# Performance work log

Measured on AMD Instinct MI355X. Metric: run time of the kernel, lower is better.

The kernel has to match this reference:

```python
import jax, jax.numpy as jnp
import numpy as np

N_NODES = 100000

def _sage_conv(x, src, dst, W_l, b_l, W_r):
    # PyG SAGEConv(aggr='mean'): out = lin_l(mean_{j in N(i)} x_j) + lin_r(x_i)
    agg = jax.ops.segment_sum(x[src], dst, num_segments=N_NODES)          # [N, F]
    cnt = jax.ops.segment_sum(jnp.ones_like(dst, dtype=x.dtype), dst,
                              num_segments=N_NODES)                        # [N]
    mean = agg / jnp.maximum(cnt, 1.0)[:, None]
    return mean @ W_l + b_l + x @ W_r

def setup_inputs() -> dict:
    key = jax.random.key(0)
    ks = jax.random.split(key, 10)
    F_in, H = 128, 16
    E, P = 1600000, 2000000
    x = jax.random.normal(ks[0], (N_NODES, F_in), dtype=jnp.float32)
    edge_index = jax.random.randint(ks[1], (2, E), 0, N_NODES, dtype=jnp.int64)
    decode_index = jax.random.randint(ks[2], (2, P), 0, N_NODES, dtype=jnp.int64)
    s1 = 1.0 / np.sqrt(F_in)
    s2 = 1.0 / np.sqrt(H)
    W1l = jax.random.uniform(ks[3], (F_in, H), jnp.float32, -s1, s1)
    b1 = jax.random.uniform(ks[4], (H,), jnp.float32, -s1, s1)
    W1r = jax.random.uniform(ks[5], (F_in, H), jnp.float32, -s1, s1)
    W2l = jax.random.uniform(ks[6], (H, H), jnp.float32, -s2, s2)
    b2 = jax.random.uniform(ks[7], (H,), jnp.float32, -s2, s2)
    W2r = jax.random.uniform(ks[8], (H, H), jnp.float32, -s2, s2)
    return {"x": x, "W1l": W1l, "b1": b1, "W1r": W1r,
            "W2l": W2l, "b2": b2, "W2r": W2r,
            "edge_index": edge_index, "decode_index": decode_index}

def reference(x, W1l, b1, W1r, W2l, b2, W2r, edge_index, decode_index):
    src, dst = edge_index[0], edge_index[1]
    h = _sage_conv(x, src, dst, W1l, b1, W1r)          # conv1
    h = jax.nn.relu(h)                                  # relu (dropout: eval -> identity)
    h = _sage_conv(h, src, dst, W2l, b2, W2r)           # conv2
    logits = jnp.sum(h[decode_index[0]] * h[decode_index[1]], axis=1)  # [P]
    return jax.nn.sigmoid(logits)
```

## Files before the change

### kernel.cpp

```cpp
#include <hip/hip_runtime.h>
#include <hip/hip_fp16.h>

#define N_NODES 100000
#define F_IN 128
#define H 16
#define NBIN 391
#define BINCAP 4608
#define ECHUNK 8192
#define QSCALE 4096.0f
#define QINV (1.0f / 4096.0f)

__device__ inline unsigned int packi16(float a, float b) {
  int ia = __float2int_rn(fminf(fmaxf(a * QSCALE, -32767.f), 32767.f));
  int ib = __float2int_rn(fminf(fmaxf(b * QSCALE, -32767.f), 32767.f));
  return (unsigned int)((ia & 0xffff) | (ib << 16));
}

__device__ inline unsigned long long pk64(unsigned int w) {
  return ((unsigned long long)((w >> 16) ^ 0x8000u) << 32)
       | (unsigned long long)((w & 0xffffu) ^ 0x8000u);
}

__global__ void __launch_bounds__(512) k_init(int* __restrict__ binCur) {
  int t = threadIdx.x;
  if (t < NBIN) binCur[t] = t * BINCAP;
}

__global__ void __launch_bounds__(512) k_front(
    const float* __restrict__ x, const float* __restrict__ W1l,
    const float* __restrict__ W1r, unsigned short* __restrict__ y1l,
    float* __restrict__ y1r,
    const int* __restrict__ src, const int* __restrict__ dst,
    int* __restrict__ binCur, int* __restrict__ recs, int E, int fillB) {
  __shared__ __align__(16) char smem[49152];
  int t = threadIdx.x;
  int b = blockIdx.x;
  if (b < fillB) {
    int* hist = (int*)smem;
    int* gbase = hist + 512;
    int* cnt2 = gbase + 512;
    hist[t] = 0;
    cnt2[t] = 0;
    __syncthreads();
    int base = b * ECHUNK;
    int rec[16], bin[16];
#pragma unroll
    for (int j = 0; j < 16; ++j) {
      int e = base + j * 512 + t;
      if (e < E) {
        int s = src[e];
        int d = dst[e];
        rec[j] = (s << 8) | (d & 255);
        bin[j] = d >> 8;
        atomicAdd(&hist[bin[j]], 1);
      } else {
        bin[j] = -1;
      }
    }
    __syncthreads();
    if (t < NBIN) {
      int c = hist[t];
      gbase[t] = (c > 0) ? atomicAdd(&binCur[t], c) : 0;
    }
    __syncthreads();
#pragma unroll
    for (int j = 0; j < 16; ++j) {
      if (bin[j] >= 0) {
        int loc = atomicAdd(&cnt2[bin[j]], 1);
        int slot = gbase[bin[j]] + loc;
        if (slot < (bin[j] + 1) * BINCAP)
          recs[slot] = rec[j];
      }
    }
  } else {
    int lb = b - fillB;
    int wid = __builtin_amdgcn_readfirstlane(t >> 6);
    int part = wid & 3;
    int g = wid >> 2;
    int ln = t & 63;
    int n = lb * 128 + g * 64 + ln;
    int nc = (n < N_NODES) ? n : (N_NODES - 1);
    float* red = (float*)smem + g * 6144;
    const float4* xr = (const float4*)(x + (size_t)nc * F_IN + part * (F_IN / 4));
    float4 xv[8];
#pragma unroll
    for (int j = 0; j < 8; ++j) xv[j] = xr[j];
    const float* Wl = W1l + part * (F_IN / 4) * H;
    const float* Wr = W1r + part * (F_IN / 4) * H;
    float al[H], ar[H];
#pragma unroll
    for (int c = 0; c < H; ++c) { al[c] = 0.f; ar[c] = 0.f; }
#pragma unroll
    for (int j = 0; j < 8; ++j) {
      float xs[4] = {xv[j].x, xv[j].y, xv[j].z, xv[j].w};
#pragma unroll
      for (int jj = 0; jj < 4; ++jj) {
        int k = j * 4 + jj;
#pragma unroll
        for (int c = 0; c < H; ++c) {
          al[c] = fmaf(xs[jj], Wl[k * H + c], al[c]);
          ar[c] = fmaf(xs[jj], Wr[k * H + c], ar[c]);
        }
      }
    }
    if (part != 0) {
      int base = (part - 1) * 2048;
#pragma unroll
      for (int c = 0; c < H; ++c) {
        red[base + c * 64 + ln] = al[c];
        red[base + (H + c) * 64 + ln] = ar[c];
      }
    }
    __syncthreads();
    if (part == 0 && n < N_NODES) {
#pragma unroll
      for (int c = 0; c < H; ++c) {
        al[c] = ((al[c] + red[c * 64 + ln]) + red[2048 + c * 64 + ln])
                + red[4096 + c * 64 + ln];
        ar[c] = ((ar[c] + red[(H + c) * 64 + ln]) + red[2048 + (H + c) * 64 + ln])
                + red[4096 + (H + c) * 64 + ln];
      }
      uint4 w0, w1;
      w0.x = packi16(al[0], al[1]);  w0.y = packi16(al[2], al[3]);
      w0.z = packi16(al[4], al[5]);  w0.w = packi16(al[6], al[7]);
      w1.x = packi16(al[8], al[9]);  w1.y = packi16(al[10], al[11]);
      w1.z = packi16(al[12], al[13]); w1.w = packi16(al[14], al[15]);
      uint4* ol = (uint4*)(y1l + (size_t)n * H);
      ol[0] = w0;
      ol[1] = w1;
      float4* orr = (float4*)(y1r + (size_t)n * H);
#pragma unroll
      for (int q = 0; q < 4; ++q)
        orr[q] = make_float4(ar[4 * q], ar[4 * q + 1], ar[4 * q + 2], ar[4 * q + 3]);
    }
  }
}

__global__ void __launch_bounds__(512) k_agg1(
    const int* __restrict__ recs, const int* __restrict__ binCur,
    const unsigned short* __restrict__ y1l, const float* __restrict__ y1r,
    const float* __restrict__ b1, const float* __restrict__ W2l,
    const float* __restrict__ W2r, unsigned short* __restrict__ z2l,
    float* __restrict__ z2r) {
  __shared__ unsigned long long acc[8][256];
  __shared__ int cnt[256];
  __shared__ float hf[16][256];
  __shared__ float w2l[256];
  __shared__ float w2r[256];
  int t = threadIdx.x;
  int b = blockIdx.x;
#pragma unroll
  for (int j = 0; j < 4; ++j) ((unsigned long long*)acc)[j * 512 + t] = 0ULL;
  if (t < 256) { cnt[t] = 0; w2l[t] = W2l[t]; }
  else         w2r[t - 256] = W2r[t - 256];
  __syncthreads();
  int rbase = b * BINCAP;
  int R = binCur[b] - rbase;
  if (R > BINCAP) R = BINCAP;
  int rr[9];
#pragma unroll
  for (int j = 0; j < 9; ++j) {
    int idx = j * 512 + t;
    rr[j] = (idx < R) ? recs[rbase + idx] : -1;
  }
  uint4 va[9], vb[9];
#pragma unroll
  for (int j = 0; j < 9; ++j) {
    int s = (rr[j] >= 0) ? (rr[j] >> 8) : 0;
    const uint4* yp = (const uint4*)(y1l + (size_t)s * H);
    va[j] = yp[0];
    vb[j] = yp[1];
  }
#pragma unroll
  for (int j = 0; j < 9; ++j) {
    if (rr[j] >= 0) {
      int nb = rr[j] & 255;
      uint4 v0 = va[j], v1 = vb[j];
      atomicAdd(&cnt[nb], 1);
      atomicAdd(&acc[0][nb], pk64(v0.x));
      atomicAdd(&acc[1][nb], pk64(v0.y));
      atomicAdd(&acc[2][nb], pk64(v0.z));
      atomicAdd(&acc[3][nb], pk64(v0.w));
      atomicAdd(&acc[4][nb], pk64(v1.x));
      atomicAdd(&acc[5][nb], pk64(v1.y));
      atomicAdd(&acc[6][nb], pk64(v1.z));
      atomicAdd(&acc[7][nb], pk64(v1.w));
    }
  }
  __syncthreads();
  int node = t >> 1;
  int half = t & 1;
  int coff = half * 8;
  int n = (b << 8) + node;
  if (n < N_NODES) {
    int dg = cnt[node];
    unsigned int bias = (unsigned int)dg << 15;
    float s = QINV / fmaxf((float)dg, 1.f);
    const float4* yrp = (const float4*)(y1r + (size_t)n * H + coff);
    float4 y0 = yrp[0], y1v = yrp[1];
    const float4* bp = (const float4*)(b1 + coff);
    float4 b0 = bp[0], b1v = bp[1];
    float yv[8] = {y0.x, y0.y, y0.z, y0.w, y1v.x, y1v.y, y1v.z, y1v.w};
    float bv[8] = {b0.x, b0.y, b0.z, b0.w, b1v.x, b1v.y, b1v.z, b1v.w};
    int ia[8];
#pragma unroll
    for (int p = 0; p < 4; ++p) {
      unsigned long long a = acc[half * 4 + p][node];
      ia[2 * p]     = (int)((unsigned int)a - bias);
      ia[2 * p + 1] = (int)((unsigned int)(a >> 32) - bias);
    }
#pragma unroll
    for (int c = 0; c < 8; ++c) {
      float h = fmaf((float)ia[c], s, bv[c] + yv[c]);
      hf[coff + c][node] = fmaxf(h, 0.f);
    }
  } else {
#pragma unroll
    for (int c = 0; c < 8; ++c) hf[coff + c][node] = 0.f;
  }
  __syncthreads();
  float zl[8], zr[8];
#pragma unroll
  for (int c = 0; c < 8; ++c) { zl[c] = 0.f; zr[c] = 0.f; }
#pragma unroll
  for (int k = 0; k < 16; ++k) {
    float hk = hf[k][node];
#pragma unroll
    for (int c = 0; c < 8; ++c) {
      zl[c] = fmaf(hk, w2l[k * 16 + coff + c], zl[c]);
      zr[c] = fmaf(hk, w2r[k * 16 + coff + c], zr[c]);
    }
  }
  if (n < N_NODES) {
    uint4 pk;
    pk.x = packi16(zl[0], zl[1]);
    pk.y = packi16(zl[2], zl[3]);
    pk.z = packi16(zl[4], zl[5]);
    pk.w = packi16(zl[6], zl[7]);
    *(uint4*)(z2l + (size_t)n * H + coff) = pk;
    float4* zp = (float4*)(z2r + (size_t)n * H + coff);
    zp[0] = make_float4(zr[0], zr[1], zr[2], zr[3]);
    zp[1] = make_float4(zr[4], zr[5], zr[6], zr[7]);
  }
}

__global__ void __launch_bounds__(512) k_agg2(
    const int* __restrict__ recs, const int* __restrict__ binCur,
    const unsigned short* __restrict__ z2l, const float* __restrict__ z2r,
    const float* __restrict__ b2, __half* __restrict__ h2) {
  __shared__ unsigned long long acc[8][256];
  __shared__ int cnt[256];
  int t = threadIdx.x;
  int b = blockIdx.x;
#pragma unroll
  for (int j = 0; j < 4; ++j) ((unsigned long long*)acc)[j * 512 + t] = 0ULL;
  if (t < 256) cnt[t] = 0;
  __syncthreads();
  int rbase = b * BINCAP;
  int R = binCur[b] - rbase;
  if (R > BINCAP) R = BINCAP;
  int rr[9];
#pragma unroll
  for (int j = 0; j < 9; ++j) {
    int idx = j * 512 + t;
    rr[j] = (idx < R) ? recs[rbase + idx] : -1;
  }
  uint4 va[9], vb[9];
#pragma unroll
  for (int j = 0; j < 9; ++j) {
    int s = (rr[j] >= 0) ? (rr[j] >> 8) : 0;
    const uint4* yp = (const uint4*)(z2l + (size_t)s * H);
    va[j] = yp[0];
    vb[j] = yp[1];
  }
#pragma unroll
  for (int j = 0; j < 9; ++j) {
    if (rr[j] >= 0) {
      int nb = rr[j] & 255;
      uint4 v0 = va[j], v1 = vb[j];
      atomicAdd(&cnt[nb], 1);
      atomicAdd(&acc[0][nb], pk64(v0.x));
      atomicAdd(&acc[1][nb], pk64(v0.y));
      atomicAdd(&acc[2][nb], pk64(v0.z));
      atomicAdd(&acc[3][nb], pk64(v0.w));
      atomicAdd(&acc[4][nb], pk64(v1.x));
      atomicAdd(&acc[5][nb], pk64(v1.y));
      atomicAdd(&acc[6][nb], pk64(v1.z));
      atomicAdd(&acc[7][nb], pk64(v1.w));
    }
  }
  __syncthreads();
  int node = t >> 1;
  int half = t & 1;
  int coff = half * 8;
  int n = (b << 8) + node;
  if (n < N_NODES) {
    int dg = cnt[node];
    unsigned int bias = (unsigned int)dg << 15;
    float s = QINV / fmaxf((float)dg, 1.f);
    const float4* zrp = (const float4*)(z2r + (size_t)n * H + coff);
    float4 z0 = zrp[0], z1 = zrp[1];
    const float4* bp = (const float4*)(b2 + coff);
    float4 b0 = bp[0], b1v = bp[1];
    float zv[8] = {z0.x, z0.y, z0.z, z0.w, z1.x, z1.y, z1.z, z1.w};
    float bv[8] = {b0.x, b0.y, b0.z, b0.w, b1v.x, b1v.y, b1v.z, b1v.w};
    int ia[8];
#pragma unroll
    for (int p = 0; p < 4; ++p) {
      unsigned long long a = acc[half * 4 + p][node];
      ia[2 * p]     = (int)((unsigned int)a - bias);
      ia[2 * p + 1] = (int)((unsigned int)(a >> 32) - bias);
    }
    float v[8];
#pragma unroll
    for (int c = 0; c < 8; ++c)
      v[c] = fmaf((float)ia[c], s, bv[c] + zv[c]);
    __half2 h0 = __floats2half2_rn(v[0], v[1]);
    __half2 h1 = __floats2half2_rn(v[2], v[3]);
    __half2 h2p = __floats2half2_rn(v[4], v[5]);
    __half2 h3 = __floats2half2_rn(v[6], v[7]);
    uint4 pk;
    pk.x = *(unsigned int*)&h0;
    pk.y = *(unsigned int*)&h1;
    pk.z = *(unsigned int*)&h2p;
    pk.w = *(unsigned int*)&h3;
    *(uint4*)(h2 + (size_t)n * H + coff) = pk;
  }
}

__device__ inline float dot8h(uint4 u, uint4 v) {
  float acc = 0.f;
  const unsigned int* uw = (const unsigned int*)&u;
  const unsigned int* vw = (const unsigned int*)&v;
#pragma unroll
  for (int j = 0; j < 4; ++j) {
    float2 a = __half22float2(*(const __half2*)&uw[j]);
    float2 b = __half22float2(*(const __half2*)&vw[j]);
    acc = fmaf(a.x, b.x, acc);
    acc = fmaf(a.y, b.y, acc);
  }
  return acc;
}

__global__ void __launch_bounds__(256) k_decode(
    const int* __restrict__ ps, const int* __restrict__ pd,
    const __half* __restrict__ h2, float* __restrict__ out, int P) {
  int t = blockIdx.x * 256 + threadIdx.x;
  int p = t * 2;
  if (p >= P) return;
  int2 av = *(const int2*)(ps + p);
  int2 bv = *(const int2*)(pd + p);
  const uint4* ha0 = (const uint4*)(h2 + (size_t)av.x * H);
  const uint4* hb0 = (const uint4*)(h2 + (size_t)bv.x * H);
  const uint4* ha1 = (const uint4*)(h2 + (size_t)av.y * H);
  const uint4* hb1 = (const uint4*)(h2 + (size_t)bv.y * H);
  uint4 u00 = ha0[0], u01 = ha0[1];
  uint4 v00 = hb0[0], v01 = hb0[1];
  uint4 u10 = ha1[0], u11 = ha1[1];
  uint4 v10 = hb1[0], v11 = hb1[1];
  float d0 = dot8h(u00, v00) + dot8h(u01, v01);
  float d1 = dot8h(u10, v10) + dot8h(u11, v11);
  float o0 = 1.f / (1.f + __expf(-d0));
  float o1 = 1.f / (1.f + __expf(-d1));
  if (p + 1 < P) {
    *(float2*)(out + p) = make_float2(o0, o1);
  } else {
    out[p] = o0;
  }
}

extern "C" void kernel_launch(void* const* d_in, const int* in_sizes, int n_in,
                              void* d_out, int out_size, void* d_ws, size_t ws_size,
                              hipStream_t stream) {
  const float* x   = (const float*)d_in[0];
  const float* W1l = (const float*)d_in[1];
  const float* b1  = (const float*)d_in[2];
  const float* W1r = (const float*)d_in[3];
  const float* W2l = (const float*)d_in[4];
  const float* b2  = (const float*)d_in[5];
  const float* W2r = (const float*)d_in[6];
  const int* ei = (const int*)d_in[7];
  const int* di = (const int*)d_in[8];
  const int E = in_sizes[7] / 2;
  const int P = in_sizes[8] / 2;

  const size_t NF = (size_t)N_NODES * H;
  unsigned short* y1l = (unsigned short*)d_ws;
  __half*         h2  = (__half*)y1l;
  unsigned short* z2l = y1l + NF;
  float*  y1r = (float*)(z2l + NF);
  float*  z2r = y1r;
  int* recs   = (int*)(y1r + NF);
  int* binCur = recs + (size_t)NBIN * BINCAP;

  const int fillB = (E + ECHUNK - 1) / ECHUNK;
  const int lin1B = (N_NODES + 127) / 128;
  const int decodeBlocks = ((P + 1) / 2 + 255) / 256;

  k_init<<<1, 512, 0, stream>>>(binCur);
  k_front<<<fillB + lin1B, 512, 0, stream>>>(x, W1l, W1r, y1l, y1r,
                                             ei, ei + E, binCur, recs, E, fillB);
  k_agg1<<<NBIN, 512, 0, stream>>>(recs, binCur, y1l, y1r, b1, W2l, W2r,
                                   z2l, z2r);
  k_agg2<<<NBIN, 512, 0, stream>>>(recs, binCur, z2l, z2r, b2, h2);
  k_decode<<<decodeBlocks, 256, 0, stream>>>(di, di + P, h2, (float*)d_out, P);
}
```

Measured before the change: 197.6 us.

## Fuse all stages into one persistent kernel with software grid barriers

Replaces the four separate stage kernels (front/bin-fill, agg1, agg2, decode) with one persistent kernel of 391 blocks that moves between stages using atomic-counter grid barriers. Edge binning and the first linear layer run as grid-stride loops within the same blocks. The register-held gather batches in the aggregation stages are processed in chunks of three to lower register pressure under the tighter launch bounds. This removes kernel launch gaps and tail effects, but relies on all 391 blocks being co-resident and limits the decode and front phases to a fixed block count.

```diff
diff --git a/kernel.cpp b/kernel.cpp
--- a/kernel.cpp
+++ b/kernel.cpp
@@ -6,7 +6,8 @@
 #define H 16
 #define NBIN 391
 #define BINCAP 4608
-#define ECHUNK 8192
+#define NBLK 391
+#define FCHUNK 4096
 #define QSCALE 4096.0f
 #define QINV (1.0f / 4096.0f)
 
@@ -21,351 +22,401 @@
        | (unsigned long long)((w & 0xffffu) ^ 0x8000u);
 }
 
-__global__ void __launch_bounds__(512) k_init(int* __restrict__ binCur) {
+__device__ inline void grid_sync(int* cnt, int* gen) {
+  __syncthreads();
+  if (threadIdx.x == 0) {
+    __threadfence();
+    int g = __hip_atomic_load(gen, __ATOMIC_RELAXED, __HIP_MEMORY_SCOPE_AGENT);
+    int v = __hip_atomic_fetch_add(cnt, 1, __ATOMIC_ACQ_REL,
+                                   __HIP_MEMORY_SCOPE_AGENT);
+    if (v == NBLK - 1) {
+      __hip_atomic_store(cnt, 0, __ATOMIC_RELAXED, __HIP_MEMORY_SCOPE_AGENT);
+      __hip_atomic_fetch_add(gen, 1, __ATOMIC_RELEASE,
+                             __HIP_MEMORY_SCOPE_AGENT);
+    } else {
+      while (__hip_atomic_load(gen, __ATOMIC_ACQUIRE,
+                               __HIP_MEMORY_SCOPE_AGENT) == g)
+        __builtin_amdgcn_s_sleep(8);
+    }
+    __threadfence();
+  }
+  __syncthreads();
+}
+
+__global__ void __launch_bounds__(1024) k_init(int* __restrict__ binCur) {
   int t = threadIdx.x;
-  if (t < NBIN) binCur[t] = t * BINCAP;
-}
-
-__global__ void __launch_bounds__(512) k_front(
+  binCur[t] = (t < 512) ? t * BINCAP : 0;
+}
+
+__global__ void __launch_bounds__(512, 4) k_mega(
     const float* __restrict__ x, const float* __restrict__ W1l,
-    const float* __restrict__ W1r, unsigned short* __restrict__ y1l,
-    float* __restrict__ y1r,
-    const int* __restrict__ src, const int* __restrict__ dst,
-    int* __restrict__ binCur, int* __restrict__ recs, int E, int fillB) {
+    const float* __restrict__ W1r, const float* __restrict__ b1,
+    const float* __restrict__ W2l, const float* __restrict__ W2r,
+    const float* __restrict__ b2, const int* __restrict__ src,
+    const int* __restrict__ dst, const int* __restrict__ ps,
+    const int* __restrict__ pd, unsigned short* y1l,
+    unsigned short* z2l, float* y1r, int* recs, int* binCur,
+    float* __restrict__ out, int E, int P) {
   __shared__ __align__(16) char smem[49152];
   int t = threadIdx.x;
   int b = blockIdx.x;
-  if (b < fillB) {
+  int* barCnt = binCur + 544;
+  int* barGen = binCur + 576;
+
+  {
     int* hist = (int*)smem;
     int* gbase = hist + 512;
     int* cnt2 = gbase + 512;
-    hist[t] = 0;
-    cnt2[t] = 0;
-    __syncthreads();
-    int base = b * ECHUNK;
-    int rec[16], bin[16];
-#pragma unroll
-    for (int j = 0; j < 16; ++j) {
-      int e = base + j * 512 + t;
-      if (e < E) {
-        int s = src[e];
-        int d = dst[e];
-        rec[j] = (s << 8) | (d & 255);
-        bin[j] = d >> 8;
-        atomicAdd(&hist[bin[j]], 1);
-      } else {
-        bin[j] = -1;
-      }
-    }
-    __syncthreads();
-    if (t < NBIN) {
-      int c = hist[t];
-      gbase[t] = (c > 0) ? atomicAdd(&binCur[t], c) : 0;
-    }
-    __syncthreads();
-#pragma unroll
-    for (int j = 0; j < 16; ++j) {
-      if (bin[j] >= 0) {
-        int loc = atomicAdd(&cnt2[bin[j]], 1);
-        int slot = gbase[bin[j]] + loc;
-        if (slot < (bin[j] + 1) * BINCAP)
-          recs[slot] = rec[j];
-      }
-    }
-  } else {
-    int lb = b - fillB;
+    int nchunks = (E + FCHUNK - 1) / FCHUNK;
+    for (int c = b; c < nchunks; c += NBLK) {
+      hist[t] = 0;
+      cnt2[t] = 0;
+      __syncthreads();
+      int base = c * FCHUNK;
+      int rec[8], bin[8];
+#pragma unroll
+      for (int j = 0; j < 8; ++j) {
+        int e = base + j * 512 + t;
+        if (e < E) {
+          int s = src[e];
+          int d = dst[e];
+          rec[j] = (s << 8) | (d & 255);
+          bin[j] = d >> 8;
+          atomicAdd(&hist[bin[j]], 1);
+        } else {
+          bin[j] = -1;
+        }
+      }
+      __syncthreads();
+      if (t < NBIN) {
+        int cc = hist[t];
+        gbase[t] = (cc > 0) ? atomicAdd(&binCur[t], cc) : 0;
+      }
+      __syncthreads();
+#pragma unroll
+      for (int j = 0; j < 8; ++j) {
+        if (bin[j] >= 0) {
+          int loc = atomicAdd(&cnt2[bin[j]], 1);
+          int slot = gbase[bin[j]] + loc;
+          if (slot < (bin[j] + 1) * BINCAP)
+            recs[slot] = rec[j];
+        }
+      }
+      __syncthreads();
+    }
+  }
+  __syncthreads();
+
+  {
     int wid = __builtin_amdgcn_readfirstlane(t >> 6);
     int part = wid & 3;
     int g = wid >> 2;
     int ln = t & 63;
-    int n = lb * 128 + g * 64 + ln;
-    int nc = (n < N_NODES) ? n : (N_NODES - 1);
     float* red = (float*)smem + g * 6144;
-    const float4* xr = (const float4*)(x + (size_t)nc * F_IN + part * (F_IN / 4));
-    float4 xv[8];
-#pragma unroll
-    for (int j = 0; j < 8; ++j) xv[j] = xr[j];
-    const float* Wl = W1l + part * (F_IN / 4) * H;
-    const float* Wr = W1r + part * (F_IN / 4) * H;
-    float al[H], ar[H];
-#pragma unroll
-    for (int c = 0; c < H; ++c) { al[c] = 0.f; ar[c] = 0.f; }
-#pragma unroll
-    for (int j = 0; j < 8; ++j) {
-      float xs[4] = {xv[j].x, xv[j].y, xv[j].z, xv[j].w};
-#pragma unroll
-      for (int jj = 0; jj < 4; ++jj) {
-        int k = j * 4 + jj;
+#pragma unroll 1
+    for (int tile = b; tile < 782; tile += NBLK) {
+      int n = tile * 128 + g * 64 + ln;
+      int nc = (n < N_NODES) ? n : (N_NODES - 1);
+      const float4* xr =
+          (const float4*)(x + (size_t)nc * F_IN + part * (F_IN / 4));
+      float4 xv[8];
+#pragma unroll
+      for (int j = 0; j < 8; ++j) xv[j] = xr[j];
+      const float* Wl = W1l + part * (F_IN / 4) * H;
+      const float* Wr = W1r + part * (F_IN / 4) * H;
+      float al[H], ar[H];
+#pragma unroll
+      for (int c = 0; c < H; ++c) { al[c] = 0.f; ar[c] = 0.f; }
+#pragma unroll
+      for (int j = 0; j < 8; ++j) {
+        float xs[4] = {xv[j].x, xv[j].y, xv[j].z, xv[j].w};
+#pragma unroll
+        for (int jj = 0; jj < 4; ++jj) {
+          int k = j * 4 + jj;
+#pragma unroll
+          for (int c = 0; c < H; ++c) {
+            al[c] = fmaf(xs[jj], Wl[k * H + c], al[c]);
+            ar[c] = fmaf(xs[jj], Wr[k * H + c], ar[c]);
+          }
+        }
+      }
+      if (part != 0) {
+        int base = (part - 1) * 2048;
 #pragma unroll
         for (int c = 0; c < H; ++c) {
-          al[c] = fmaf(xs[jj], Wl[k * H + c], al[c]);
-          ar[c] = fmaf(xs[jj], Wr[k * H + c], ar[c]);
-        }
-      }
-    }
-    if (part != 0) {
-      int base = (part - 1) * 2048;
-#pragma unroll
-      for (int c = 0; c < H; ++c) {
-        red[base + c * 64 + ln] = al[c];
-        red[base + (H + c) * 64 + ln] = ar[c];
-      }
-    }
+          red[base + c * 64 + ln] = al[c];
+          red[base + (H + c) * 64 + ln] = ar[c];
+        }
+      }
+      __syncthreads();
+      if (part == 0 && n < N_NODES) {
+#pragma unroll
+        for (int c = 0; c < H; ++c) {
+          al[c] = ((al[c] + red[c * 64 + ln]) + red[2048 + c * 64 + ln])
+                  + red[4096 + c * 64 + ln];
+          ar[c] = ((ar[c] + red[(H + c) * 64 + ln])
+                   + red[2048 + (H + c) * 64 + ln])
+                  + red[4096 + (H + c) * 64 + ln];
+        }
+        uint4 w0, w1;
+        w0.x = packi16(al[0], al[1]);  w0.y = packi16(al[2], al[3]);
+        w0.z = packi16(al[4], al[5]);  w0.w = packi16(al[6], al[7]);
+        w1.x = packi16(al[8], al[9]);  w1.y = packi16(al[10], al[11]);
+        w1.z = packi16(al[12], al[13]); w1.w = packi16(al[14], al[15]);
+        uint4* ol = (uint4*)(y1l + (size_t)n * H);
+        ol[0] = w0;
+        ol[1] = w1;
+        float4* orr = (float4*)(y1r + (size_t)n * H);
+#pragma unroll
+        for (int q = 0; q < 4; ++q)
+          orr[q] = make_float4(ar[4 * q], ar[4 * q + 1], ar[4 * q + 2],
+                               ar[4 * q + 3]);
+      }
+      __syncthreads();
+    }
+  }
+  grid_sync(barCnt, barGen);
+
+  {
+    unsigned long long (*acc)[256] = (unsigned long long (*)[256])smem;
+    int* cnt = (int*)(smem + 16384);
+    float (*hf)[256] = (float (*)[256])(smem + 17408);
+    float* w2l = (float*)(smem + 33792);
+    float* w2r = (float*)(smem + 34816);
+#pragma unroll
+    for (int j = 0; j < 4; ++j) ((unsigned long long*)acc)[j * 512 + t] = 0ULL;
+    if (t < 256) { cnt[t] = 0; w2l[t] = W2l[t]; }
+    else         w2r[t - 256] = W2r[t - 256];
     __syncthreads();
-    if (part == 0 && n < N_NODES) {
-#pragma unroll
-      for (int c = 0; c < H; ++c) {
-        al[c] = ((al[c] + red[c * 64 + ln]) + red[2048 + c * 64 + ln])
-                + red[4096 + c * 64 + ln];
-        ar[c] = ((ar[c] + red[(H + c) * 64 + ln]) + red[2048 + (H + c) * 64 + ln])
-                + red[4096 + (H + c) * 64 + ln];
-      }
-      uint4 w0, w1;
-      w0.x = packi16(al[0], al[1]);  w0.y = packi16(al[2], al[3]);
-      w0.z = packi16(al[4], al[5]);  w0.w = packi16(al[6], al[7]);
-      w1.x = packi16(al[8], al[9]);  w1.y = packi16(al[10], al[11]);
-      w1.z = packi16(al[12], al[13]); w1.w = packi16(al[14], al[15]);
-      uint4* ol = (uint4*)(y1l + (size_t)n * H);
-      ol[0] = w0;
-      ol[1] = w1;
-      float4* orr = (float4*)(y1r + (size_t)n * H);
-#pragma unroll
-      for (int q = 0; q < 4; ++q)
-        orr[q] = make_float4(ar[4 * q], ar[4 * q + 1], ar[4 * q + 2], ar[4 * q + 3]);
-    }
-  }
-}
-
-__global__ void __launch_bounds__(512) k_agg1(
-    const int* __restrict__ recs, const int* __restrict__ binCur,
-    const unsigned short* __restrict__ y1l, const float* __restrict__ y1r,
-    const float* __restrict__ b1, const float* __restrict__ W2l,
-    const float* __restrict__ W2r, unsigned short* __restrict__ z2l,
-    float* __restrict__ z2r) {
-  __shared__ unsigned long long acc[8][256];
-  __shared__ int cnt[256];
-  __shared__ float hf[16][256];
-  __shared__ float w2l[256];
-  __shared__ float w2r[256];
-  int t = threadIdx.x;
-  int b = blockIdx.x;
-#pragma unroll
-  for (int j = 0; j < 4; ++j) ((unsigned long long*)acc)[j * 512 + t] = 0ULL;
-  if (t < 256) { cnt[t] = 0; w2l[t] = W2l[t]; }
-  else         w2r[t - 256] = W2r[t - 256];
-  __syncthreads();
-  int rbase = b * BINCAP;
-  int R = binCur[b] - rbase;
-  if (R > BINCAP) R = BINCAP;
-  int rr[9];
-#pragma unroll
-  for (int j = 0; j < 9; ++j) {
-    int idx = j * 512 + t;
-    rr[j] = (idx < R) ? recs[rbase + idx] : -1;
-  }
-  uint4 va[9], vb[9];
-#pragma unroll
-  for (int j = 0; j < 9; ++j) {
-    int s = (rr[j] >= 0) ? (rr[j] >> 8) : 0;
-    const uint4* yp = (const uint4*)(y1l + (size_t)s * H);
-    va[j] = yp[0];
-    vb[j] = yp[1];
-  }
-#pragma unroll
-  for (int j = 0; j < 9; ++j) {
-    if (rr[j] >= 0) {
-      int nb = rr[j] & 255;
-      uint4 v0 = va[j], v1 = vb[j];
-      atomicAdd(&cnt[nb], 1);
-      atomicAdd(&acc[0][nb], pk64(v0.x));
-      atomicAdd(&acc[1][nb], pk64(v0.y));
-      atomicAdd(&acc[2][nb], pk64(v0.z));
-      atomicAdd(&acc[3][nb], pk64(v0.w));
-      atomicAdd(&acc[4][nb], pk64(v1.x));
-      atomicAdd(&acc[5][nb], pk64(v1.y));
-      atomicAdd(&acc[6][nb], pk64(v1.z));
-      atomicAdd(&acc[7][nb], pk64(v1.w));
-    }
-  }
-  __syncthreads();
-  int node = t >> 1;
-  int half = t & 1;
-  int coff = half * 8;
-  int n = (b << 8) + node;
-  if (n < N_NODES) {
-    int dg = cnt[node];
-    unsigned int bias = (unsigned int)dg << 15;
-    float s = QINV / fmaxf((float)dg, 1.f);
-    const float4* yrp = (const float4*)(y1r + (size_t)n * H + coff);
-    float4 y0 = yrp[0], y1v = yrp[1];
-    const float4* bp = (const float4*)(b1 + coff);
-    float4 b0 = bp[0], b1v = bp[1];
-    float yv[8] = {y0.x, y0.y, y0.z, y0.w, y1v.x, y1v.y, y1v.z, y1v.w};
-    float bv[8] = {b0.x, b0.y, b0.z, b0.w, b1v.x, b1v.y, b1v.z, b1v.w};
-    int ia[8];
-#pragma unroll
-    for (int p = 0; p < 4; ++p) {
-      unsigned long long a = acc[half * 4 + p][node];
-      ia[2 * p]     = (int)((unsigned int)a - bias);
-      ia[2 * p + 1] = (int)((unsigned int)(a >> 32) - bias);
-    }
-#pragma unroll
-    for (int c = 0; c < 8; ++c) {
-      float h = fmaf((float)ia[c], s, bv[c] + yv[c]);
-      hf[coff + c][node] = fmaxf(h, 0.f);
-    }
-  } else {
-#pragma unroll
-    for (int c = 0; c < 8; ++c) hf[coff + c][node] = 0.f;
-  }
-  __syncthreads();
-  float zl[8], zr[8];
-#pragma unroll
-  for (int c = 0; c < 8; ++c) { zl[c] = 0.f; zr[c] = 0.f; }
-#pragma unroll
-  for (int k = 0; k < 16; ++k) {
-    float hk = hf[k][node];
-#pragma unroll
-    for (int c = 0; c < 8; ++c) {
-      zl[c] = fmaf(hk, w2l[k * 16 + coff + c], zl[c]);
-      zr[c] = fmaf(hk, w2r[k * 16 + coff + c], zr[c]);
-    }
-  }
-  if (n < N_NODES) {
-    uint4 pk;
-    pk.x = packi16(zl[0], zl[1]);
-    pk.y = packi16(zl[2], zl[3]);
-    pk.z = packi16(zl[4], zl[5]);
-    pk.w = packi16(zl[6], zl[7]);
-    *(uint4*)(z2l + (size_t)n * H + coff) = pk;
-    float4* zp = (float4*)(z2r + (size_t)n * H + coff);
-    zp[0] = make_float4(zr[0], zr[1], zr[2], zr[3]);
-    zp[1] = make_float4(zr[4], zr[5], zr[6], zr[7]);
-  }
-}
-
-__global__ void __launch_bounds__(512) k_agg2(
-    const int* __restrict__ recs, const int* __restrict__ binCur,
-    const unsigned short* __restrict__ z2l, const float* __restrict__ z2r,
-    const float* __restrict__ b2, __half* __restrict__ h2) {
-  __shared__ unsigned long long acc[8][256];
-  __shared__ int cnt[256];
-  int t = threadIdx.x;
-  int b = blockIdx.x;
-#pragma unroll
-  for (int j = 0; j < 4; ++j) ((unsigned long long*)acc)[j * 512 + t] = 0ULL;
-  if (t < 256) cnt[t] = 0;
-  __syncthreads();
-  int rbase = b * BINCAP;
-  int R = binCur[b] - rbase;
-  if (R > BINCAP) R = BINCAP;
-  int rr[9];
-#pragma unroll
-  for (int j = 0; j < 9; ++j) {
-    int idx = j * 512 + t;
-    rr[j] = (idx < R) ? recs[rbase + idx] : -1;
-  }
-  uint4 va[9], vb[9];
-#pragma unroll
-  for (int j = 0; j < 9; ++j) {
-    int s = (rr[j] >= 0) ? (rr[j] >> 8) : 0;
-    const uint4* yp = (const uint4*)(z2l + (size_t)s * H);
-    va[j] = yp[0];
-    vb[j] = yp[1];
-  }
-#pragma unroll
-  for (int j = 0; j < 9; ++j) {
-    if (rr[j] >= 0) {
-      int nb = rr[j] & 255;
-      uint4 v0 = va[j], v1 = vb[j];
-      atomicAdd(&cnt[nb], 1);
-      atomicAdd(&acc[0][nb], pk64(v0.x));
-      atomicAdd(&acc[1][nb], pk64(v0.y));
-      atomicAdd(&acc[2][nb], pk64(v0.z));
-      atomicAdd(&acc[3][nb], pk64(v0.w));
-      atomicAdd(&acc[4][nb], pk64(v1.x));
-      atomicAdd(&acc[5][nb], pk64(v1.y));
-      atomicAdd(&acc[6][nb], pk64(v1.z));
-      atomicAdd(&acc[7][nb], pk64(v1.w));
-    }
-  }
-  __syncthreads();
-  int node = t >> 1;
-  int half = t & 1;
-  int coff = half * 8;
-  int n = (b << 8) + node;
-  if (n < N_NODES) {
-    int dg = cnt[node];
-    unsigned int bias = (unsigned int)dg << 15;
-    float s = QINV / fmaxf((float)dg, 1.f);
-    const float4* zrp = (const float4*)(z2r + (size_t)n * H + coff);
-    float4 z0 = zrp[0], z1 = zrp[1];
-    const float4* bp = (const float4*)(b2 + coff);
-    float4 b0 = bp[0], b1v = bp[1];
-    float zv[8] = {z0.x, z0.y, z0.z, z0.w, z1.x, z1.y, z1.z, z1.w};
-    float bv[8] = {b0.x, b0.y, b0.z, b0.w, b1v.x, b1v.y, b1v.z, b1v.w};
-    int ia[8];
-#pragma unroll
-    for (int p = 0; p < 4; ++p) {
-      unsigned long long a = acc[half * 4 + p][node];
-      ia[2 * p]     = (int)((unsigned int)a - bias);
-      ia[2 * p + 1] = (int)((unsigned int)(a >> 32) - bias);
-    }
-    float v[8];
-#pragma unroll
-    for (int c = 0; c < 8; ++c)
-      v[c] = fmaf((float)ia[c], s, bv[c] + zv[c]);
-    __half2 h0 = __floats2half2_rn(v[0], v[1]);
-    __half2 h1 = __floats2half2_rn(v[2], v[3]);
-    __half2 h2p = __floats2half2_rn(v[4], v[5]);
-    __half2 h3 = __floats2half2_rn(v[6], v[7]);
-    uint4 pk;
-    pk.x = *(unsigned int*)&h0;
-    pk.y = *(unsigned int*)&h1;
-    pk.z = *(unsigned int*)&h2p;
-    pk.w = *(unsigned int*)&h3;
-    *(uint4*)(h2 + (size_t)n * H + coff) = pk;
-  }
-}
-
-__device__ inline float dot8h(uint4 u, uint4 v) {
-  float acc = 0.f;
-  const unsigned int* uw = (const unsigned int*)&u;
-  const unsigned int* vw = (const unsigned int*)&v;
-#pragma unroll
-  for (int j = 0; j < 4; ++j) {
-    float2 a = __half22float2(*(const __half2*)&uw[j]);
-    float2 b = __half22float2(*(const __half2*)&vw[j]);
-    acc = fmaf(a.x, b.x, acc);
-    acc = fmaf(a.y, b.y, acc);
-  }
-  return acc;
-}
-
-__global__ void __launch_bounds__(256) k_decode(
-    const int* __restrict__ ps, const int* __restrict__ pd,
-    const __half* __restrict__ h2, float* __restrict__ out, int P) {
-  int t = blockIdx.x * 256 + threadIdx.x;
-  int p = t * 2;
-  if (p >= P) return;
-  int2 av = *(const int2*)(ps + p);
-  int2 bv = *(const int2*)(pd + p);
-  const uint4* ha0 = (const uint4*)(h2 + (size_t)av.x * H);
-  const uint4* hb0 = (const uint4*)(h2 + (size_t)bv.x * H);
-  const uint4* ha1 = (const uint4*)(h2 + (size_t)av.y * H);
-  const uint4* hb1 = (const uint4*)(h2 + (size_t)bv.y * H);
-  uint4 u00 = ha0[0], u01 = ha0[1];
-  uint4 v00 = hb0[0], v01 = hb0[1];
-  uint4 u10 = ha1[0], u11 = ha1[1];
-  uint4 v10 = hb1[0], v11 = hb1[1];
-  float d0 = dot8h(u00, v00) + dot8h(u01, v01);
-  float d1 = dot8h(u10, v10) + dot8h(u11, v11);
-  float o0 = 1.f / (1.f + __expf(-d0));
-  float o1 = 1.f / (1.f + __expf(-d1));
-  if (p + 1 < P) {
-    *(float2*)(out + p) = make_float2(o0, o1);
-  } else {
-    out[p] = o0;
+    int rbase = b * BINCAP;
+    int R = binCur[b] - rbase;
+    if (R > BINCAP) R = BINCAP;
+#pragma unroll 1
+    for (int c0 = 0; c0 < 9; c0 += 3) {
+      int rc[3];
+      uint4 va[3], vb[3];
+#pragma unroll
+      for (int jj = 0; jj < 3; ++jj) {
+        int idx = (c0 + jj) * 512 + t;
+        rc[jj] = (idx < R) ? recs[rbase + idx] : -1;
+      }
+#pragma unroll
+      for (int jj = 0; jj < 3; ++jj) {
+        int s = (rc[jj] >= 0) ? (rc[jj] >> 8) : 0;
+        const uint4* yp = (const uint4*)(y1l + (size_t)s * H);
+        va[jj] = yp[0];
+        vb[jj] = yp[1];
+      }
+#pragma unroll
+      for (int jj = 0; jj < 3; ++jj) {
+        if (rc[jj] >= 0) {
+          int nb = rc[jj] & 255;
+          atomicAdd(&cnt[nb], 1);
+          atomicAdd(&acc[0][nb], pk64(va[jj].x));
+          atomicAdd(&acc[1][nb], pk64(va[jj].y));
+          atomicAdd(&acc[2][nb], pk64(va[jj].z));
+          atomicAdd(&acc[3][nb], pk64(va[jj].w));
+          atomicAdd(&acc[4][nb], pk64(vb[jj].x));
+          atomicAdd(&acc[5][nb], pk64(vb[jj].y));
+          atomicAdd(&acc[6][nb], pk64(vb[jj].z));
+          atomicAdd(&acc[7][nb], pk64(vb[jj].w));
+        }
+      }
+    }
+    __syncthreads();
+    int node = t >> 1;
+    int half = t & 1;
+    int coff = half * 8;
+    int n = (b << 8) + node;
+    if (n < N_NODES) {
+      int dg = cnt[node];
+      unsigned int bias = (unsigned int)dg << 15;
+      float s = QINV / fmaxf((float)dg, 1.f);
+      const float4* yrp = (const float4*)(y1r + (size_t)n * H + coff);
+      float4 y0 = yrp[0], y1v = yrp[1];
+      const float4* bp = (const float4*)(b1 + coff);
+      float4 b0 = bp[0], b1v = bp[1];
+      float yv[8] = {y0.x, y0.y, y0.z, y0.w, y1v.x, y1v.y, y1v.z, y1v.w};
+      float bv[8] = {b0.x, b0.y, b0.z, b0.w, b1v.x, b1v.y, b1v.z, b1v.w};
+      int ia[8];
+#pragma unroll
+      for (int p = 0; p < 4; ++p) {
+        unsigned long long a = acc[half * 4 + p][node];
+        ia[2 * p]     = (int)((unsigned int)a - bias);
+        ia[2 * p + 1] = (int)((unsigned int)(a >> 32) - bias);
+      }
+#pragma unroll
+      for (int c = 0; c < 8; ++c) {
+        float h = fmaf((float)ia[c], s, bv[c] + yv[c]);
+        hf[coff + c][node] = fmaxf(h, 0.f);
+      }
+    } else {
+#pragma unroll
+      for (int c = 0; c < 8; ++c) hf[coff + c][node] = 0.f;
+    }
+    __syncthreads();
+    float zl[8], zr[8];
+#pragma unroll
+    for (int c = 0; c < 8; ++c) { zl[c] = 0.f; zr[c] = 0.f; }
+#pragma unroll
+    for (int k = 0; k < 16; ++k) {
+      float hk = hf[k][node];
+#pragma unroll
+      for (int c = 0; c < 8; ++c) {
+        zl[c] = fmaf(hk, w2l[k * 16 + coff + c], zl[c]);
+        zr[c] = fmaf(hk, w2r[k * 16 + coff + c], zr[c]);
+      }
+    }
+    if (n < N_NODES) {
+      uint4 pk;
+      pk.x = packi16(zl[0], zl[1]);
+      pk.y = packi16(zl[2], zl[3]);
+      pk.z = packi16(zl[4], zl[5]);
+      pk.w = packi16(zl[6], zl[7]);
+      *(uint4*)(z2l + (size_t)n * H + coff) = pk;
+      float4* zp = (float4*)(y1r + (size_t)n * H + coff);
+      zp[0] = make_float4(zr[0], zr[1], zr[2], zr[3]);
+      zp[1] = make_float4(zr[4], zr[5], zr[6], zr[7]);
+    }
+  }
+  grid_sync(barCnt, barGen);
+
+  {
+    unsigned long long (*acc)[256] = (unsigned long long (*)[256])smem;
+    int* cnt = (int*)(smem + 16384);
+#pragma unroll
+    for (int j = 0; j < 4; ++j) ((unsigned long long*)acc)[j * 512 + t] = 0ULL;
+    if (t < 256) cnt[t] = 0;
+    __syncthreads();
+    int rbase = b * BINCAP;
+    int R = binCur[b] - rbase;
+    if (R > BINCAP) R = BINCAP;
+#pragma unroll 1
+    for (int c0 = 0; c0 < 9; c0 += 3) {
+      int rc[3];
+      uint4 va[3], vb[3];
+#pragma unroll
+      for (int jj = 0; jj < 3; ++jj) {
+        int idx = (c0 + jj) * 512 + t;
+        rc[jj] = (idx < R) ? recs[rbase + idx] : -1;
+      }
+#pragma unroll
+      for (int jj = 0; jj < 3; ++jj) {
+        int s = (rc[jj] >= 0) ? (rc[jj] >> 8) : 0;
+        const uint4* yp = (const uint4*)(z2l + (size_t)s * H);
+        va[jj] = yp[0];
+        vb[jj] = yp[1];
+      }
+#pragma unroll
+      for (int jj = 0; jj < 3; ++jj) {
+        if (rc[jj] >= 0) {
+          int nb = rc[jj] & 255;
+          atomicAdd(&cnt[nb], 1);
+          atomicAdd(&acc[0][nb], pk64(va[jj].x));
+          atomicAdd(&acc[1][nb], pk64(va[jj].y));
+          atomicAdd(&acc[2][nb], pk64(va[jj].z));
+          atomicAdd(&acc[3][nb], pk64(va[jj].w));
+          atomicAdd(&acc[4][nb], pk64(vb[jj].x));
+          atomicAdd(&acc[5][nb], pk64(vb[jj].y));
+          atomicAdd(&acc[6][nb], pk64(vb[jj].z));
+          atomicAdd(&acc[7][nb], pk64(vb[jj].w));
+        }
+      }
+    }
+    __syncthreads();
+    int node = t >> 1;
+    int half = t & 1;
+    int coff = half * 8;
+    int n = (b << 8) + node;
+    if (n < N_NODES) {
+      int dg = cnt[node];
+      unsigned int bias = (unsigned int)dg << 15;
+      float s = QINV / fmaxf((float)dg, 1.f);
+      const float4* zrp = (const float4*)(y1r + (size_t)n * H + coff);
+      float4 z0 = zrp[0], z1 = zrp[1];
+      const float4* bp = (const float4*)(b2 + coff);
+      float4 b0 = bp[0], b1v = bp[1];
+      float zv[8] = {z0.x, z0.y, z0.z, z0.w, z1.x, z1.y, z1.z, z1.w};
+      float bv[8] = {b0.x, b0.y, b0.z, b0.w, b1v.x, b1v.y, b1v.z, b1v.w};
+      int ia[8];
+#pragma unroll
+      for (int p = 0; p < 4; ++p) {
+        unsigned long long a = acc[half * 4 + p][node];
+        ia[2 * p]     = (int)((unsigned int)a - bias);
+        ia[2 * p + 1] = (int)((unsigned int)(a >> 32) - bias);
+      }
+      float v[8];
+#pragma unroll
+      for (int c = 0; c < 8; ++c)
+        v[c] = fmaf((float)ia[c], s, bv[c] + zv[c]);
+      __half2 h0 = __floats2half2_rn(v[0], v[1]);
+      __half2 h1 = __floats2half2_rn(v[2], v[3]);
+      __half2 hh2 = __floats2half2_rn(v[4], v[5]);
+      __half2 h3 = __floats2half2_rn(v[6], v[7]);
+      uint4 pk;
+      pk.x = *(unsigned int*)&h0;
+      pk.y = *(unsigned int*)&h1;
+      pk.z = *(unsigned int*)&hh2;
+      pk.w = *(unsigned int*)&h3;
+      *(uint4*)((__half*)y1l + (size_t)n * H + coff) = pk;
+    }
+  }
+  grid_sync(barCnt, barGen);
+
+  {
+    const __half* h2 = (const __half*)y1l;
+    const int tp = NBLK * 512;
+    for (int u = b * 512 + t; 2 * u < P; u += tp) {
+      int p = 2 * u;
+      int2 av = *(const int2*)(ps + p);
+      int2 bv = *(const int2*)(pd + p);
+      const uint4* ha0 = (const uint4*)(h2 + (size_t)av.x * H);
+      const uint4* hb0 = (const uint4*)(h2 + (size_t)bv.x * H);
+      const uint4* ha1 = (const uint4*)(h2 + (size_t)av.y * H);
+      const uint4* hb1 = (const uint4*)(h2 + (size_t)bv.y * H);
+      uint4 u00 = ha0[0], u01 = ha0[1];
+      uint4 v00 = hb0[0], v01 = hb0[1];
+      uint4 u10 = ha1[0], u11 = ha1[1];
+      uint4 v10 = hb1[0], v11 = hb1[1];
+      float d0 = 0.f, d1 = 0.f;
+      const unsigned int* uw;
+      const unsigned int* vw;
+      uw = (const unsigned int*)&u00; vw = (const unsigned int*)&v00;
+#pragma unroll
+      for (int j = 0; j < 4; ++j) {
+        float2 a = __half22float2(*(const __half2*)&uw[j]);
+        float2 bb = __half22float2(*(const __half2*)&vw[j]);
+        d0 = fmaf(a.x, bb.x, d0); d0 = fmaf(a.y, bb.y, d0);
+      }
+      uw = (const unsigned int*)&u01; vw = (const unsigned int*)&v01;
+#pragma unroll
+      for (int j = 0; j < 4; ++j) {
+        float2 a = __half22float2(*(const __half2*)&uw[j]);
+        float2 bb = __half22float2(*(const __half2*)&vw[j]);
+        d0 = fmaf(a.x, bb.x, d0); d0 = fmaf(a.y, bb.y, d0);
+      }
+      uw = (const unsigned int*)&u10; vw = (const unsigned int*)&v10;
+#pragma unroll
+      for (int j = 0; j < 4; ++j) {
+        float2 a = __half22float2(*(const __half2*)&uw[j]);
+        float2 bb = __half22float2(*(const __half2*)&vw[j]);
+        d1 = fmaf(a.x, bb.x, d1); d1 = fmaf(a.y, bb.y, d1);
+      }
+      uw = (const unsigned int*)&u11; vw = (const unsigned int*)&v11;
+#pragma unroll
+      for (int j = 0; j < 4; ++j) {
+        float2 a = __half22float2(*(const __half2*)&uw[j]);
+        float2 bb = __half22float2(*(const __half2*)&vw[j]);
+        d1 = fmaf(a.x, bb.x, d1); d1 = fmaf(a.y, bb.y, d1);
+      }
+      float o0 = 1.f / (1.f + __expf(-d0));
+      float o1 = 1.f / (1.f + __expf(-d1));
+      if (p + 1 < P) {
+        *(float2*)(out + p) = make_float2(o0, o1);
+      } else {
+        out[p] = o0;
+      }
+    }
   }
 }
 
@@ -386,22 +437,14 @@
 
   const size_t NF = (size_t)N_NODES * H;
   unsigned short* y1l = (unsigned short*)d_ws;
-  __half*         h2  = (__half*)y1l;
   unsigned short* z2l = y1l + NF;
   float*  y1r = (float*)(z2l + NF);
-  float*  z2r = y1r;
   int* recs   = (int*)(y1r + NF);
   int* binCur = recs + (size_t)NBIN * BINCAP;
 
-  const int fillB = (E + ECHUNK - 1) / ECHUNK;
-  const int lin1B = (N_NODES + 127) / 128;
-  const int decodeBlocks = ((P + 1) / 2 + 255) / 256;
-
-  k_init<<<1, 512, 0, stream>>>(binCur);
-  k_front<<<fillB + lin1B, 512, 0, stream>>>(x, W1l, W1r, y1l, y1r,
-                                             ei, ei + E, binCur, recs, E, fillB);
-  k_agg1<<<NBIN, 512, 0, stream>>>(recs, binCur, y1l, y1r, b1, W2l, W2r,
-                                   z2l, z2r);
-  k_agg2<<<NBIN, 512, 0, stream>>>(recs, binCur, z2l, z2r, b2, h2);
-  k_decode<<<decodeBlocks, 256, 0, stream>>>(di, di + P, h2, (float*)d_out, P);
-}
+  k_init<<<1, 1024, 0, stream>>>(binCur);
+  k_mega<<<NBLK, 512, 0, stream>>>(x, W1l, W1r, b1, W2l, W2r, b2,
+                                   ei, ei + E, di, di + P,
+                                   y1l, z2l, y1r, recs, binCur,
+                                   (float*)d_out, E, P);
+}
```

Measured after the change: 518.8 us. 2.63x slower.
